# Optimization experiments

Measured on AMD Instinct MI355X. Metric: run time of the kernel, lower is better.

Reference implementation:

```python
import jax, jax.numpy as jnp
import numpy as np

B, N, D, E = 4, 16384, 128, 1048576  # batch, nodes/graph, hidden, total edges


def setup_inputs() -> dict:
    key = jax.random.key(0)
    k0, k1, k2, k3, k4, k5, k6 = jax.random.split(key, 7)
    x = jax.random.normal(k0, (B, N, D), dtype=jnp.float32)
    W = jax.random.normal(k1, (D, D), dtype=jnp.float32) * 0.05  # 'random_normal' init
    b = jax.random.normal(k2, (D,), dtype=jnp.float32) * 0.05
    edge_b = jax.random.randint(k3, (E,), 0, B, dtype=jnp.int32)
    edge_row = jax.random.randint(k4, (E,), 0, N, dtype=jnp.int32)
    edge_col = jax.random.randint(k5, (E,), 0, N, dtype=jnp.int32)
    edge_vals = jax.random.uniform(k6, (E,), dtype=jnp.float32)
    return {"x": x, "W": W, "b": b, "edge_b": edge_b, "edge_row": edge_row,
            "edge_col": edge_col, "edge_vals": edge_vals, "k": 2}


def reference(x, W, b, edge_b, edge_row, edge_col, edge_vals, k):
    # adj is a batched sparse [B, N, N]; edges stored as (batch, row, col, val) COO.
    seg_row = edge_b * N + edge_row  # flattened destination id in [0, B*N)
    # in_degrees = sum_j |adj[b, i, j]|
    deg = jax.ops.segment_sum(jnp.abs(edge_vals), seg_row, num_segments=B * N)
    deg = deg.reshape(B, N)
    norm = jnp.power(deg + 1e-6, -0.5)[..., None]          # [B, N, 1]
    norm_k = jnp.power(norm, k)                             # computed but unused (faithful to source)
    support = jnp.einsum('bnd,de->bne', x, W)               # x @ W
    y = (support * norm).reshape(B * N, D)                  # pre-normalized features
    # SpMM: out[b, i] = sum_{(b,i,j)} adj_val * y[b, j]
    msgs = y[edge_b * N + edge_col] * edge_vals[:, None]    # [E, D] gather + scale
    agg = jax.ops.segment_sum(msgs, seg_row, num_segments=B * N).reshape(B, N, D)
    return jax.nn.relu(agg * norm + b)
```

## Files before the change

kernel.cpp:

```cpp
#include <hip/hip_runtime.h>
#include <stdint.h>

#define B_ 4
#define N_ 16384
#define D_ 128
#define E_ 1048576
#define BN_ 65536
#define NBKT 256
#define NBLK 256
#define CAP  6144

typedef __attribute__((ext_vector_type(8))) short short8;
typedef __attribute__((ext_vector_type(4))) float floatx4;

static constexpr size_t OFF_Y      = 0;
static constexpr size_t OFF_PACK1  = 16777216;
static constexpr size_t OFF_GBKT   = OFF_PACK1 + 12582912;
static constexpr size_t OFF_NORM   = OFF_GBKT + 1024;
static constexpr size_t OFF_WH     = OFF_NORM + 262144;
static constexpr size_t OFF_WL     = OFF_WH + 32768;

__device__ __forceinline__ uint32_t rne16(uint32_t u) {
    return (u + 0x7FFFu + ((u >> 16) & 1u)) >> 16;
}
__device__ __forceinline__ void bf16split(float f, uint16_t& h, uint16_t& l) {
    uint32_t hb = rne16(__float_as_uint(f));
    h = (uint16_t)hb;
    float r = f - __uint_as_float(hb << 16);
    l = (uint16_t)rne16(__float_as_uint(r));
}

__global__ __launch_bounds__(1024, 2) void k_scatter(const int* __restrict__ eb,
                                                     const int* __restrict__ er,
                                                     const int* __restrict__ ec,
                                                     const float* __restrict__ ev,
                                                     const float* __restrict__ Wg,
                                                     uint32_t* __restrict__ gbkt,
                                                     uint2* __restrict__ pack1,
                                                     uint16_t* __restrict__ WhG,
                                                     uint16_t* __restrict__ WlG) {
    __shared__ uint32_t h[NBKT];
    int t = threadIdx.x;
    if (t < NBKT) h[t] = 0;
    if (blockIdx.x < 16) {
        int g = blockIdx.x * 1024 + t;
        float w = Wg[g];
        uint16_t hh, ll;
        bf16split(w, hh, ll);
        int k = g >> 7, n = g & 127;
        int o = ((k >> 3) * 128 + n) * 8 + (k & 7);
        WhG[o] = hh;
        WlG[o] = ll;
    }
    __syncthreads();
    int vbase = blockIdx.x * 1024 + t;
    int4   b4 = ((const int4*)eb)[vbase];
    int4   r4 = ((const int4*)er)[vbase];
    int4   c4 = ((const int4*)ec)[vbase];
    float4 v4 = ((const float4*)ev)[vbase];
    uint32_t k0 = (uint32_t)(b4.x * N_ + r4.x);
    uint32_t k1 = (uint32_t)(b4.y * N_ + r4.y);
    uint32_t k2 = (uint32_t)(b4.z * N_ + r4.z);
    uint32_t k3 = (uint32_t)(b4.w * N_ + r4.w);
    atomicAdd(&h[k0 >> 8], 1u);
    atomicAdd(&h[k1 >> 8], 1u);
    atomicAdd(&h[k2 >> 8], 1u);
    atomicAdd(&h[k3 >> 8], 1u);
    __syncthreads();
    if (t < NBKT) {
        uint32_t c = h[t];
        uint32_t base = c ? atomicAdd(&gbkt[t], c) : 0u;
        h[t] = base;
    }
    __syncthreads();
    {
        uint32_t off = atomicAdd(&h[k0 >> 8], 1u);
        pack1[(size_t)(k0 >> 8) * CAP + off] =
            make_uint2(((k0 & 255u) << 14) | (uint32_t)c4.x, __float_as_uint(v4.x));
    }
    {
        uint32_t off = atomicAdd(&h[k1 >> 8], 1u);
        pack1[(size_t)(k1 >> 8) * CAP + off] =
            make_uint2(((k1 & 255u) << 14) | (uint32_t)c4.y, __float_as_uint(v4.y));
    }
    {
        uint32_t off = atomicAdd(&h[k2 >> 8], 1u);
        pack1[(size_t)(k2 >> 8) * CAP + off] =
            make_uint2(((k2 & 255u) << 14) | (uint32_t)c4.z, __float_as_uint(v4.z));
    }
    {
        uint32_t off = atomicAdd(&h[k3 >> 8], 1u);
        pack1[(size_t)(k3 >> 8) * CAP + off] =
            make_uint2(((k3 & 255u) << 14) | (uint32_t)c4.w, __float_as_uint(v4.w));
    }
}

__global__ __launch_bounds__(1024) void k_deg(const uint32_t* __restrict__ gbkt,
                                              const uint2* __restrict__ pack1,
                                              float* __restrict__ norm) {
    __shared__ float dsum[NBKT];
    int t = threadIdx.x;
    int bkt = blockIdx.x;
    if (t < NBKT) dsum[t] = 0.f;
    __syncthreads();
    uint32_t cnt = gbkt[bkt];
    size_t bstart = (size_t)bkt * CAP;
    for (uint32_t i = t; i < cnt; i += 1024) {
        uint2 p = pack1[bstart + i];
        atomicAdd(&dsum[p.x >> 14], fabsf(__uint_as_float(p.y)));
    }
    __syncthreads();
    if (t < NBKT) norm[bkt * NBKT + t] = rsqrtf(dsum[t] + 1e-6f);
}

__global__ __launch_bounds__(256) void k_matmul_mfma(const float* __restrict__ x,
                                                     const uint16_t* __restrict__ WhG,
                                                     const uint16_t* __restrict__ WlG,
                                                     const float* __restrict__ norm,
                                                     uint32_t* __restrict__ ybf) {
    __shared__ short WhS[16384];
    __shared__ short WlS[16384];
    __shared__ short XhS[4096];
    __shared__ short XlS[4096];
    __shared__ float normS[32];
    int tid = threadIdx.x;
    int row0 = blockIdx.x * 32;

    {
        const uint4* whg = (const uint4*)WhG;
        const uint4* wlg = (const uint4*)WlG;
        uint4* whs = (uint4*)WhS;
        uint4* wls = (uint4*)WlS;
#pragma unroll
        for (int i = 0; i < 8; ++i) {
            whs[i * 256 + tid] = whg[i * 256 + tid];
            wls[i * 256 + tid] = wlg[i * 256 + tid];
        }
    }
#pragma unroll
    for (int cc = 0; cc < 2; ++cc) {
        int c = cc * 256 + tid;
        int m = c & 31, kk = c >> 5;
        const float4* xp = (const float4*)(x + (size_t)(row0 + m) * D_ + kk * 8);
        float4 f0 = xp[0], f1 = xp[1];
        union { short8 v; uint16_t s[8]; } uh, ul;
        bf16split(f0.x, uh.s[0], ul.s[0]); bf16split(f0.y, uh.s[1], ul.s[1]);
        bf16split(f0.z, uh.s[2], ul.s[2]); bf16split(f0.w, uh.s[3], ul.s[3]);
        bf16split(f1.x, uh.s[4], ul.s[4]); bf16split(f1.y, uh.s[5], ul.s[5]);
        bf16split(f1.z, uh.s[6], ul.s[6]); bf16split(f1.w, uh.s[7], ul.s[7]);
        ((short8*)XhS)[c] = uh.v;
        ((short8*)XlS)[c] = ul.v;
    }
    if (tid < 32) normS[tid] = norm[row0 + tid];
    __syncthreads();

    int lane = tid & 63;
    int wv = tid >> 6;
    int quad = lane >> 4;
    int l15 = lane & 15;
    int wcol0 = wv * 32;
    floatx4 acc[2][2] = {};
    const short8* Xh8 = (const short8*)XhS;
    const short8* Xl8 = (const short8*)XlS;
    const short8* Wh8 = (const short8*)WhS;
    const short8* Wl8 = (const short8*)WlS;
#pragma unroll
    for (int ks = 0; ks < 4; ++ks) {
        int kkq = ks * 4 + quad;
        short8 ah0 = Xh8[kkq * 32 + l15];
        short8 ah1 = Xh8[kkq * 32 + 16 + l15];
        short8 al0 = Xl8[kkq * 32 + l15];
        short8 al1 = Xl8[kkq * 32 + 16 + l15];
        short8 bh0 = Wh8[kkq * 128 + wcol0 + l15];
        short8 bh1 = Wh8[kkq * 128 + wcol0 + 16 + l15];
        short8 bl0 = Wl8[kkq * 128 + wcol0 + l15];
        short8 bl1 = Wl8[kkq * 128 + wcol0 + 16 + l15];
        acc[0][0] = __builtin_amdgcn_mfma_f32_16x16x32_bf16(ah0, bh0, acc[0][0], 0, 0, 0);
        acc[0][1] = __builtin_amdgcn_mfma_f32_16x16x32_bf16(ah0, bh1, acc[0][1], 0, 0, 0);
        acc[1][0] = __builtin_amdgcn_mfma_f32_16x16x32_bf16(ah1, bh0, acc[1][0], 0, 0, 0);
        acc[1][1] = __builtin_amdgcn_mfma_f32_16x16x32_bf16(ah1, bh1, acc[1][1], 0, 0, 0);
        acc[0][0] = __builtin_amdgcn_mfma_f32_16x16x32_bf16(ah0, bl0, acc[0][0], 0, 0, 0);
        acc[0][1] = __builtin_amdgcn_mfma_f32_16x16x32_bf16(ah0, bl1, acc[0][1], 0, 0, 0);
        acc[1][0] = __builtin_amdgcn_mfma_f32_16x16x32_bf16(ah1, bl0, acc[1][0], 0, 0, 0);
        acc[1][1] = __builtin_amdgcn_mfma_f32_16x16x32_bf16(ah1, bl1, acc[1][1], 0, 0, 0);
        acc[0][0] = __builtin_amdgcn_mfma_f32_16x16x32_bf16(al0, bh0, acc[0][0], 0, 0, 0);
        acc[0][1] = __builtin_amdgcn_mfma_f32_16x16x32_bf16(al0, bh1, acc[0][1], 0, 0, 0);
        acc[1][0] = __builtin_amdgcn_mfma_f32_16x16x32_bf16(al1, bh0, acc[1][0], 0, 0, 0);
        acc[1][1] = __builtin_amdgcn_mfma_f32_16x16x32_bf16(al1, bh1, acc[1][1], 0, 0, 0);
    }

#pragma unroll
    for (int rt = 0; rt < 2; ++rt) {
#pragma unroll
        for (int ct = 0; ct < 2; ++ct) {
            floatx4 v = acc[rt][ct];
            int rbase = rt * 16 + quad * 4;
            int cp = (wcol0 + ct * 16) / 2 + (l15 >> 1);
#pragma unroll
            for (int r = 0; r < 4; ++r) {
                float mine = v[r] * normS[rbase + r];
                float oth = __shfl_xor(mine, 1, 64);
                uint32_t a = __float_as_uint((lane & 1) ? oth : mine);
                uint32_t b = __float_as_uint((lane & 1) ? mine : oth);
                uint32_t packed = rne16(a) | (rne16(b) << 16);
                bool doit = ((lane & 1) == 0) ? (r < 2) : (r >= 2);
                if (doit)
                    ybf[(size_t)(row0 + rbase + r) * 64 + cp] = packed;
            }
        }
    }
}

__device__ __forceinline__ void fma8(float* acc, float v, uint4 u) {
    acc[0] = fmaf(v, __uint_as_float(u.x << 16), acc[0]);
    acc[1] = fmaf(v, __uint_as_float(u.x & 0xFFFF0000u), acc[1]);
    acc[2] = fmaf(v, __uint_as_float(u.y << 16), acc[2]);
    acc[3] = fmaf(v, __uint_as_float(u.y & 0xFFFF0000u), acc[3]);
    acc[4] = fmaf(v, __uint_as_float(u.z << 16), acc[4]);
    acc[5] = fmaf(v, __uint_as_float(u.z & 0xFFFF0000u), acc[5]);
    acc[6] = fmaf(v, __uint_as_float(u.w << 16), acc[6]);
    acc[7] = fmaf(v, __uint_as_float(u.w & 0xFFFF0000u), acc[7]);
}

__global__ __launch_bounds__(1024, 2) void k_spmm(const uint32_t* __restrict__ gbkt,
                                                  const uint2* __restrict__ pack1,
                                                  const uint4* __restrict__ y4,
                                                  const float* __restrict__ norm,
                                                  const float* __restrict__ bias,
                                                  float* __restrict__ out) {
    __shared__ uint2    srt[CAP];
    __shared__ uint32_t cnt[NBKT];
    __shared__ uint32_t scn[NBKT];
    __shared__ uint32_t rcur[NBKT];
    int t = threadIdx.x;
    int blk = blockIdx.x;
    int xcd = blk & 7;
    int bkt = ((xcd & 3) << 6) | ((xcd >> 2) << 5) | (blk >> 3);
    if (t < NBKT) cnt[t] = 0;
    __syncthreads();
    uint32_t n = gbkt[bkt];
    size_t base = (size_t)bkt * CAP;
    for (uint32_t i = t; i < n; i += 1024) {
        uint2 p = pack1[base + i];
        atomicAdd(&cnt[p.x >> 14], 1u);
    }
    __syncthreads();
    if (t < NBKT) scn[t] = cnt[t];
    __syncthreads();
    for (int off = 1; off < NBKT; off <<= 1) {
        uint32_t a = 0;
        if (t < NBKT && t >= off) a = scn[t - off];
        __syncthreads();
        if (t < NBKT) scn[t] += a;
        __syncthreads();
    }
    if (t < NBKT) rcur[t] = scn[t] - cnt[t];
    __syncthreads();
    for (uint32_t i = t; i < n; i += 1024) {
        uint2 p = pack1[base + i];
        uint32_t pos = atomicAdd(&rcur[p.x >> 14], 1u);
        srt[pos] = p;
    }
    __syncthreads();

    int wv = t >> 6;
    int lane = t & 63;
    int esub = lane >> 4;
    int chunk = lane & 15;
    uint32_t colbase = (uint32_t)(bkt >> 6) << 14;
#pragma unroll 1
    for (int i = 0; i < 16; ++i) {
        int nl = wv * 16 + i;
        uint32_t end = scn[nl];
        uint32_t e = end - cnt[nl];
        float acc[8] = {0.f,0.f,0.f,0.f,0.f,0.f,0.f,0.f};
        for (; e + 8 <= end; e += 8) {
            uint2 p0 = srt[e + esub];
            uint2 p1 = srt[e + 4 + esub];
            uint4 u0 = y4[(size_t)(colbase | (p0.x & 0x3FFFu)) * 16 + chunk];
            uint4 u1 = y4[(size_t)(colbase | (p1.x & 0x3FFFu)) * 16 + chunk];
            fma8(acc, __uint_as_float(p0.y), u0);
            fma8(acc, __uint_as_float(p1.y), u1);
        }
        for (; e + 4 <= end; e += 4) {
            uint2 p = srt[e + esub];
            uint4 u = y4[(size_t)(colbase | (p.x & 0x3FFFu)) * 16 + chunk];
            fma8(acc, __uint_as_float(p.y), u);
        }
        if (e < end) {
            uint32_t idx = e + esub;
            bool act = idx < end;
            uint2 p = srt[act ? idx : (end - 1)];
            uint4 u = y4[(size_t)(colbase | (p.x & 0x3FFFu)) * 16 + chunk];
            float v = act ? __uint_as_float(p.y) : 0.f;
            fma8(acc, v, u);
        }
#pragma unroll
        for (int j = 0; j < 8; ++j) {
            acc[j] += __shfl_xor(acc[j], 16, 64);
            acc[j] += __shfl_xor(acc[j], 32, 64);
        }
        if (esub < 2) {
            int node = bkt * NBKT + nl;
            float nm = norm[node];
            float4 bb = ((const float4*)bias)[chunk * 2 + esub];
            float4 o;
            o.x = fmaxf(fmaf(acc[esub * 4 + 0], nm, bb.x), 0.f);
            o.y = fmaxf(fmaf(acc[esub * 4 + 1], nm, bb.y), 0.f);
            o.z = fmaxf(fmaf(acc[esub * 4 + 2], nm, bb.z), 0.f);
            o.w = fmaxf(fmaf(acc[esub * 4 + 3], nm, bb.w), 0.f);
            ((float4*)out)[(size_t)node * 32 + chunk * 2 + esub] = o;
        }
    }
}

extern "C" void kernel_launch(void* const* d_in, const int* in_sizes, int n_in,
                              void* d_out, int out_size, void* d_ws, size_t ws_size,
                              hipStream_t stream) {
    const float* x  = (const float*)d_in[0];
    const float* W  = (const float*)d_in[1];
    const float* bi = (const float*)d_in[2];
    const int* eb   = (const int*)d_in[3];
    const int* er   = (const int*)d_in[4];
    const int* ec   = (const int*)d_in[5];
    const float* ev = (const float*)d_in[6];
    float* out = (float*)d_out;

    char* ws = (char*)d_ws;
    uint32_t* ybf    = (uint32_t*)(ws + OFF_Y);
    uint2*    pack1  = (uint2*)(ws + OFF_PACK1);
    uint32_t* gbkt   = (uint32_t*)(ws + OFF_GBKT);
    float*    norm   = (float*)(ws + OFF_NORM);
    uint16_t* WhG    = (uint16_t*)(ws + OFF_WH);
    uint16_t* WlG    = (uint16_t*)(ws + OFF_WL);

    hipMemsetAsync(gbkt, 0, NBKT * sizeof(uint32_t), stream);
    k_scatter<<<NBLK, 1024, 0, stream>>>(eb, er, ec, ev, W, gbkt, pack1, WhG, WlG);
    k_deg    <<<NBKT, 1024, 0, stream>>>(gbkt, pack1, norm);
    k_matmul_mfma<<<BN_ / 32, 256, 0, stream>>>(x, WhG, WlG, norm, ybf);
    k_spmm   <<<NBKT, 1024, 0, stream>>>(gbkt, pack1, (const uint4*)ybf, norm, bi, out);
}
```

Measured before the change: 181.0 us.

## Split each SpMM bucket across two blocks by node half and unroll gather deeper

The SpMM launch doubles to 512 blocks. Each block takes one half (128 nodes) of a 256-node bucket, filters that bucket's edges by half, and counting-sorts only its share into a smaller shared buffer. This halves the shared memory per block and gives more parallelism and occupancy on the GPU. The cost is that each bucket's packed edge list is read twice from global memory. The inner gather loop also unrolls to 16 edges per iteration so more loads are in flight.

Result: no change. 183.1 us (+1.2%).

```diff
diff --git a/kernel.cpp b/kernel.cpp
--- a/kernel.cpp
+++ b/kernel.cpp
@@ -9,6 +9,7 @@
 #define NBKT 256
 #define NBLK 256
 #define CAP  6144
+#define CAPH 3072
 
 typedef __attribute__((ext_vector_type(8))) short short8;
 typedef __attribute__((ext_vector_type(4))) float floatx4;
@@ -228,38 +229,45 @@
                                                   const float* __restrict__ norm,
                                                   const float* __restrict__ bias,
                                                   float* __restrict__ out) {
-    __shared__ uint2    srt[CAP];
-    __shared__ uint32_t cnt[NBKT];
-    __shared__ uint32_t scn[NBKT];
-    __shared__ uint32_t rcur[NBKT];
+    __shared__ uint2    srt[CAPH];
+    __shared__ uint32_t cnt[128];
+    __shared__ uint32_t scn[128];
+    __shared__ uint32_t rcur[128];
     int t = threadIdx.x;
     int blk = blockIdx.x;
     int xcd = blk & 7;
-    int bkt = ((xcd & 3) << 6) | ((xcd >> 2) << 5) | (blk >> 3);
-    if (t < NBKT) cnt[t] = 0;
+    int batch = xcd & 3;
+    int half = xcd >> 2;
+    int j = blk >> 3;
+    int bkt = batch * 64 + j;
+    if (t < 128) cnt[t] = 0;
     __syncthreads();
     uint32_t n = gbkt[bkt];
     size_t base = (size_t)bkt * CAP;
     for (uint32_t i = t; i < n; i += 1024) {
         uint2 p = pack1[base + i];
-        atomicAdd(&cnt[p.x >> 14], 1u);
-    }
-    __syncthreads();
-    if (t < NBKT) scn[t] = cnt[t];
-    __syncthreads();
-    for (int off = 1; off < NBKT; off <<= 1) {
+        uint32_t nl = p.x >> 14;
+        if ((int)(nl >> 7) == half) atomicAdd(&cnt[nl & 127], 1u);
+    }
+    __syncthreads();
+    if (t < 128) scn[t] = cnt[t];
+    __syncthreads();
+    for (int off = 1; off < 128; off <<= 1) {
         uint32_t a = 0;
-        if (t < NBKT && t >= off) a = scn[t - off];
+        if (t < 128 && t >= off) a = scn[t - off];
         __syncthreads();
-        if (t < NBKT) scn[t] += a;
+        if (t < 128) scn[t] += a;
         __syncthreads();
     }
-    if (t < NBKT) rcur[t] = scn[t] - cnt[t];
+    if (t < 128) rcur[t] = scn[t] - cnt[t];
     __syncthreads();
     for (uint32_t i = t; i < n; i += 1024) {
         uint2 p = pack1[base + i];
-        uint32_t pos = atomicAdd(&rcur[p.x >> 14], 1u);
-        srt[pos] = p;
+        uint32_t nl = p.x >> 14;
+        if ((int)(nl >> 7) == half) {
+            uint32_t pos = atomicAdd(&rcur[nl & 127], 1u);
+            srt[pos] = p;
+        }
     }
     __syncthreads();
 
@@ -267,20 +275,26 @@
     int lane = t & 63;
     int esub = lane >> 4;
     int chunk = lane & 15;
-    uint32_t colbase = (uint32_t)(bkt >> 6) << 14;
+    uint32_t colbase = (uint32_t)batch << 14;
 #pragma unroll 1
-    for (int i = 0; i < 16; ++i) {
-        int nl = wv * 16 + i;
+    for (int i = 0; i < 8; ++i) {
+        int nl = wv * 8 + i;
         uint32_t end = scn[nl];
         uint32_t e = end - cnt[nl];
         float acc[8] = {0.f,0.f,0.f,0.f,0.f,0.f,0.f,0.f};
-        for (; e + 8 <= end; e += 8) {
-            uint2 p0 = srt[e + esub];
-            uint2 p1 = srt[e + 4 + esub];
-            uint4 u0 = y4[(size_t)(colbase | (p0.x & 0x3FFFu)) * 16 + chunk];
-            uint4 u1 = y4[(size_t)(colbase | (p1.x & 0x3FFFu)) * 16 + chunk];
-            fma8(acc, __uint_as_float(p0.y), u0);
-            fma8(acc, __uint_as_float(p1.y), u1);
+        for (; e + 16 <= end; e += 16) {
+            uint2 pa = srt[e + esub];
+            uint2 pb = srt[e + 4 + esub];
+            uint2 pc = srt[e + 8 + esub];
+            uint2 pd = srt[e + 12 + esub];
+            uint4 ua = y4[(size_t)(colbase | (pa.x & 0x3FFFu)) * 16 + chunk];
+            uint4 ub = y4[(size_t)(colbase | (pb.x & 0x3FFFu)) * 16 + chunk];
+            uint4 uc = y4[(size_t)(colbase | (pc.x & 0x3FFFu)) * 16 + chunk];
+            uint4 ud = y4[(size_t)(colbase | (pd.x & 0x3FFFu)) * 16 + chunk];
+            fma8(acc, __uint_as_float(pa.y), ua);
+            fma8(acc, __uint_as_float(pb.y), ub);
+            fma8(acc, __uint_as_float(pc.y), uc);
+            fma8(acc, __uint_as_float(pd.y), ud);
         }
         for (; e + 4 <= end; e += 4) {
             uint2 p = srt[e + esub];
@@ -296,12 +310,12 @@
             fma8(acc, v, u);
         }
 #pragma unroll
-        for (int j = 0; j < 8; ++j) {
-            acc[j] += __shfl_xor(acc[j], 16, 64);
-            acc[j] += __shfl_xor(acc[j], 32, 64);
+        for (int jj = 0; jj < 8; ++jj) {
+            acc[jj] += __shfl_xor(acc[jj], 16, 64);
+            acc[jj] += __shfl_xor(acc[jj], 32, 64);
         }
         if (esub < 2) {
-            int node = bkt * NBKT + nl;
+            int node = bkt * NBKT + half * 128 + nl;
             float nm = norm[node];
             float4 bb = ((const float4*)bias)[chunk * 2 + esub];
             float4 o;
@@ -338,5 +352,5 @@
     k_scatter<<<NBLK, 1024, 0, stream>>>(eb, er, ec, ev, W, gbkt, pack1, WhG, WlG);
     k_deg    <<<NBKT, 1024, 0, stream>>>(gbkt, pack1, norm);
     k_matmul_mfma<<<BN_ / 32, 256, 0, stream>>>(x, WhG, WlG, norm, ybf);
-    k_spmm   <<<NBKT, 1024, 0, stream>>>(gbkt, pack1, (const uint4*)ybf, norm, bi, out);
-}
+    k_spmm   <<<512, 1024, 0, stream>>>(gbkt, pack1, (const uint4*)ybf, norm, bi, out);
+}
```
